# Kernel tuning notes

Hardware: AMD Instinct MI355X
Metric: run time of the kernel (lower is better)

## Reference

```python
import jax, jax.numpy as jnp
import numpy as np

N_NODES = 50000
N_EDGES = 1_600_000
D_IN, D_HID, D_OUT = 512, 256, 64


def setup_inputs() -> dict:
    key = jax.random.key(0)
    ks = jax.random.split(key, 8)
    x = jax.random.normal(ks[0], (N_NODES, D_IN), dtype=jnp.float32)
    edge_rows = jax.random.randint(ks[1], (N_EDGES,), 0, N_NODES, dtype=jnp.int32)
    edge_cols = jax.random.randint(ks[2], (N_EDGES,), 0, N_NODES, dtype=jnp.int32)
    # normalized adjacency values (e.g. D^-1/2 A D^-1/2 entries)
    edge_vals = jax.random.uniform(ks[3], (N_EDGES,), dtype=jnp.float32)
    W1 = jax.random.normal(ks[4], (D_IN, D_HID), dtype=jnp.float32) * (1.0 / np.sqrt(D_IN))
    b1 = jnp.zeros((D_HID,), dtype=jnp.float32)
    W2 = jax.random.normal(ks[5], (D_HID, D_OUT), dtype=jnp.float32) * (1.0 / np.sqrt(D_HID))
    b2 = jnp.zeros((D_OUT,), dtype=jnp.float32)
    return {"x": x, "edge_rows": edge_rows, "edge_cols": edge_cols,
            "edge_vals": edge_vals, "W1": W1, "b1": b1, "W2": W2, "b2": b2}


def _spmm(rows, cols, vals, h):
    # out[r] = sum_{e: rows[e]==r} vals[e] * h[cols[e]]
    msgs = vals[:, None] * h[cols]          # [E, d] gather
    return jax.ops.segment_sum(msgs, rows, num_segments=N_NODES)


def reference(x, edge_rows, edge_cols, edge_vals, W1, b1, W2, b2):
    h = x @ W1 + b1                          # W1(x)
    h = _spmm(edge_rows, edge_cols, edge_vals, h)  # sparse.mm(A_hat, h)
    h = jax.nn.relu(h)                       # relu; dropout is identity in eval
    h = h @ W2 + b2                           # W2(h)
    out = _spmm(edge_rows, edge_cols, edge_vals, h)
    return out
```

## Files before the change

kernel.cpp:

```cpp
#include <hip/hip_runtime.h>
#include <hip/hip_bf16.h>

constexpr int NN = 50000;
constexpr int NE = 1600000;
constexpr int DI = 512;
constexpr int DH = 256;
constexpr int DO = 64;

constexpr int NC = NN * 16;
constexpr int G1_BLOCKS = ((NN + 127) / 128) * (DH / 128);
constexpr int SC_BLOCKS = 2048;
constexpr int SCAN_BLOCKS = (NN + 1023) / 1024;
constexpr int E4_CAP = NE + NN * 16 + 64;

typedef __attribute__((ext_vector_type(8))) short short8;
typedef __attribute__((ext_vector_type(4))) float f32x4;

__device__ inline ushort f2b(float f) {
    uint u = __float_as_uint(f);
    u += 0x7fffu + ((u >> 16) & 1u);
    return (ushort)(u >> 16);
}
__device__ inline float b2f(ushort u) {
    return __uint_as_float((uint)u << 16);
}
__device__ inline void gload16(const void* g, void* l) {
    __builtin_amdgcn_global_load_lds(
        (const __attribute__((address_space(1))) unsigned int*)g,
        (__attribute__((address_space(3))) unsigned int*)l, 16, 0, 0);
}


__global__ void k_prep(const float* __restrict__ X, ushort* __restrict__ Xb,
                       const float* __restrict__ W1, ushort* __restrict__ w1bT,
                       const int* __restrict__ er, const int* __restrict__ ec,
                       int* __restrict__ counts2) {
    const int bid = blockIdx.x;
    const int tid = threadIdx.x;
    if (bid < 1024) {
        const float4* x4 = (const float4*)X;
        ushort4* o4 = (ushort4*)Xb;
        const int stride = 1024 * 256;
        for (int i = bid * 256 + tid; i < NN * DI / 4; i += stride) {
            float4 v = x4[i];
            o4[i] = make_ushort4(f2b(v.x), f2b(v.y), f2b(v.z), f2b(v.w));
        }
        for (int i = bid * 256 + tid; i < DI * DH; i += stride) {
            int n = i >> 9, k = i & 511;
            w1bT[i] = f2b(W1[(size_t)k * DH + n]);
        }
    } else {
        const int4* r4 = (const int4*)er;
        const int4* c4 = (const int4*)ec;
        const int stride = 1024 * 256;
        for (int i = (bid - 1024) * 256 + tid; i < NE / 4; i += stride) {
            int4 r = r4[i];
            int4 c = c4[i];
            atomicAdd(&counts2[(r.x << 4) | (c.x >> 12)], 1);
            atomicAdd(&counts2[(r.y << 4) | (c.y >> 12)], 1);
            atomicAdd(&counts2[(r.z << 4) | (c.z >> 12)], 1);
            atomicAdd(&counts2[(r.w << 4) | (c.w >> 12)], 1);
        }
    }
}


__global__ __launch_bounds__(1024) void k_scanA(const int* __restrict__ counts2,
                                                int* __restrict__ rp,
                                                int* __restrict__ partials) {
    const int t = threadIdx.x;
    const int r = blockIdx.x * 1024 + t;
    int s = 0;
    if (r < NN) {
        const int4* c4 = (const int4*)(counts2 + (size_t)r * 16);
        int4 a = c4[0], b = c4[1], c = c4[2], d = c4[3];
        s = a.x + a.y + a.z + a.w + b.x + b.y + b.z + b.w
          + c.x + c.y + c.z + c.w + d.x + d.y + d.z + d.w;
        s = (s + 15) & ~15;
    }
    __shared__ int buf[1024];
    buf[t] = s;
    __syncthreads();
    for (int off = 1; off < 1024; off <<= 1) {
        int v = (t >= off) ? buf[t - off] : 0;
        __syncthreads();
        buf[t] += v;
        __syncthreads();
    }
    if (r < NN) rp[r] = buf[t] - s;
    if (t == 1023) partials[blockIdx.x] = buf[1023];
}

__global__ __launch_bounds__(64) void k_scanB(int* __restrict__ partials,
                                              int* __restrict__ rp) {
    __shared__ int buf[64];
    int t = threadIdx.x;
    int v = (t < SCAN_BLOCKS) ? partials[t] : 0;
    buf[t] = v;
    __syncthreads();
    for (int off = 1; off < 64; off <<= 1) {
        int x = (t >= off) ? buf[t - off] : 0;
        __syncthreads();
        buf[t] += x;
        __syncthreads();
    }
    if (t < SCAN_BLOCKS) partials[t] = buf[t] - v;
    if (t == 63) rp[NN] = buf[63];
}

__global__ __launch_bounds__(1024) void k_scanC(const int* __restrict__ counts2,
                                                int* __restrict__ rp,
                                                int* __restrict__ cur2,
                                                const int* __restrict__ partials,
                                                const float* __restrict__ W2,
                                                ushort* __restrict__ w2bT) {
    const int t = threadIdx.x;
    const int r = blockIdx.x * 1024 + t;
    if (r < NN) {
        const int off = partials[blockIdx.x];
        const int base = rp[r] + off;
        rp[r] = base;
        const int4* c4 = (const int4*)(counts2 + (size_t)r * 16);
        int4 ca = c4[0], cb = c4[1], cc = c4[2], cd = c4[3];
        int cnt[16] = {ca.x, ca.y, ca.z, ca.w, cb.x, cb.y, cb.z, cb.w,
                       cc.x, cc.y, cc.z, cc.w, cd.x, cd.y, cd.z, cd.w};
        int out[16];
        int rs = 0;
        #pragma unroll
        for (int b = 0; b < 16; ++b) { out[b] = base + rs; rs += cnt[b]; }
        int4* o4 = (int4*)(cur2 + (size_t)r * 16);
        o4[0] = make_int4(out[0],  out[1],  out[2],  out[3]);
        o4[1] = make_int4(out[4],  out[5],  out[6],  out[7]);
        o4[2] = make_int4(out[8],  out[9],  out[10], out[11]);
        o4[3] = make_int4(out[12], out[13], out[14], out[15]);
    }
    if (blockIdx.x == 0) {
        for (int i = t; i < DH * DO; i += 1024) {
            int n = i >> 8, k = i & 255;
            w2bT[i] = f2b(W2[(size_t)k * DO + n]);
        }
    }
}


__global__ __launch_bounds__(256, 4) void k_gemm1(const ushort* __restrict__ Xb,
                                                  const ushort* __restrict__ w1bT,
                                                  const float* __restrict__ B,
                                                  ushort* __restrict__ H) {
    __shared__ ushort As[128 * 32];
    __shared__ ushort Bs[128 * 32];
    const int bid = blockIdx.x;
    const int bm = (bid >> 1) * 128;
    const int bn = (bid & 1) * 128;
    const int tid = threadIdx.x;
    const int wid = tid >> 6, lane = tid & 63;
    const int wm = wid >> 1, wn = wid & 1;
    const int lr = lane & 15, lg = lane >> 4;

    f32x4 acc[4][4];
    #pragma unroll
    for (int i = 0; i < 4; ++i)
        #pragma unroll
        for (int j = 0; j < 4; ++j)
            acc[i][j] = (f32x4){0.f, 0.f, 0.f, 0.f};

    for (int kt = 0; kt < DI; kt += 32) {
        #pragma unroll
        for (int c = 0; c < 2; ++c) {
            int i = c * 256 + tid;
            int row = i >> 2, slot = i & 3;
            const ushort* g = Xb + (size_t)(bm + row) * DI + kt + slot * 8;
            gload16(g, As + (size_t)(c * 256 + wid * 64) * 8);
        }
        #pragma unroll
        for (int c = 0; c < 2; ++c) {
            int i = c * 256 + tid;
            int row = i >> 2, slot = i & 3;
            const ushort* g = w1bT + (size_t)(bn + row) * DI + kt + slot * 8;
            gload16(g, Bs + (size_t)(c * 256 + wid * 64) * 8);
        }
        __syncthreads();

        short8 a[4], b[4];
        #pragma unroll
        for (int f = 0; f < 4; ++f) {
            a[f] = *(short8*)&As[(wm * 64 + f * 16 + lr) * 32 + lg * 8];
            b[f] = *(short8*)&Bs[(wn * 64 + f * 16 + lr) * 32 + lg * 8];
        }
        #pragma unroll
        for (int i = 0; i < 4; ++i)
            #pragma unroll
            for (int j = 0; j < 4; ++j)
                acc[i][j] = __builtin_amdgcn_mfma_f32_16x16x32_bf16(a[i], b[j], acc[i][j], 0, 0, 0);
        __syncthreads();
    }

    #pragma unroll
    for (int i = 0; i < 4; ++i) {
        int r0 = bm + wm * 64 + i * 16 + lg * 4;
        #pragma unroll
        for (int j = 0; j < 4; ++j) {
            int col = bn + wn * 64 + j * 16 + lr;
            float bias = B[col];
            #pragma unroll
            for (int e = 0; e < 4; ++e) {
                int r = r0 + e;
                if (r < NN) H[(size_t)r * DH + col] = f2b(acc[i][j][e] + bias);
            }
        }
    }
}


__global__ __launch_bounds__(256) void k_scatter(const int* __restrict__ er,
                                                 const int* __restrict__ ec,
                                                 const float* __restrict__ ev,
                                                 int* __restrict__ cur2,
                                                 uint* __restrict__ e4) {
    const int g = blockIdx.x & 7;
    const int lo = g * (NN / 8), hi = lo + (NN / 8);
    const int4* r4 = (const int4*)er;
    for (int q = (blockIdx.x >> 3) * 256 + (int)threadIdx.x; q < NE / 4;
         q += (SC_BLOCKS / 8) * 256) {
        int4 r = r4[q];
        #pragma unroll
        for (int e = 0; e < 4; ++e) {
            int rr = (e == 0) ? r.x : (e == 1) ? r.y : (e == 2) ? r.z : r.w;
            if (rr >= lo && rr < hi) {
                int c = ec[q * 4 + e];
                float v = ev[q * 4 + e];
                int p = atomicAdd(&cur2[(rr << 4) | (c >> 12)], 1);
                e4[p] = (uint)c | ((uint)f2b(v) << 16);
            }
        }
    }
}


__global__ __launch_bounds__(256) void k_srg(const int* __restrict__ rp,
                                             const uint* __restrict__ e4,
                                             const ushort* __restrict__ H,
                                             const ushort* __restrict__ w2bT,
                                             const float* __restrict__ B2,
                                             ushort* __restrict__ H2) {
    __shared__ ushort hs[16][264];
    const int tid = threadIdx.x;
    const int w = tid >> 6, lane = tid & 63;
    const int half = lane >> 5;
    const int dl = lane & 31;
    const ushort* gbase = H + dl * 8;
    const uint4* eq = (const uint4*)e4;

    #pragma unroll
    for (int q = 0; q < 4; ++q) {
        const int r = blockIdx.x * 16 + w * 4 + q;
        const int s = rp[r], e = rp[r + 1];
        float a[8] = {0.f, 0.f, 0.f, 0.f, 0.f, 0.f, 0.f, 0.f};

        int qi = s >> 2;
        uint4 q0 = eq[qi], q1 = eq[qi + 1], q2 = eq[qi + 2], q3 = eq[qi + 3];
        for (int i = s; i < e; i += 16) {
            uint u[8];
            u[0] = half ? q0.y : q0.x;  u[1] = half ? q0.w : q0.z;
            u[2] = half ? q1.y : q1.x;  u[3] = half ? q1.w : q1.z;
            u[4] = half ? q2.y : q2.x;  u[5] = half ? q2.w : q2.z;
            u[6] = half ? q3.y : q3.x;  u[7] = half ? q3.w : q3.z;
            uint4 hw[8];
            #pragma unroll
            for (int k = 0; k < 8; ++k)
                hw[k] = *(const uint4*)(gbase + (size_t)(u[k] & 0xffffu) * DH);
            qi += 4;
            q0 = eq[qi]; q1 = eq[qi + 1]; q2 = eq[qi + 2]; q3 = eq[qi + 3];
            #pragma unroll
            for (int k = 0; k < 8; ++k) {
                float v = __uint_as_float(u[k] & 0xffff0000u);
                uint w0 = hw[k].x, w1 = hw[k].y, w2 = hw[k].z, w3 = hw[k].w;
                a[0] += v * __uint_as_float(w0 << 16);
                a[1] += v * __uint_as_float(w0 & 0xffff0000u);
                a[2] += v * __uint_as_float(w1 << 16);
                a[3] += v * __uint_as_float(w1 & 0xffff0000u);
                a[4] += v * __uint_as_float(w2 << 16);
                a[5] += v * __uint_as_float(w2 & 0xffff0000u);
                a[6] += v * __uint_as_float(w3 << 16);
                a[7] += v * __uint_as_float(w3 & 0xffff0000u);
            }
        }
        #pragma unroll
        for (int d = 0; d < 8; ++d) a[d] += __shfl_xor(a[d], 32);
        if (half == 0) {
            short8 o;
            #pragma unroll
            for (int d = 0; d < 8; ++d) o[d] = (short)f2b(fmaxf(a[d], 0.f));
            *(short8*)&hs[w * 4 + q][dl * 8] = o;
        }
    }
    __syncthreads();

    const int lr = lane & 15, lg = lane >> 4;
    f32x4 acc = (f32x4){0.f, 0.f, 0.f, 0.f};
    #pragma unroll
    for (int kt = 0; kt < DH; kt += 32) {
        short8 af = *(short8*)&hs[lr][kt + lg * 8];
        short8 bf = *(const short8*)(w2bT + (size_t)(w * 16 + lr) * DH + kt + lg * 8);
        acc = __builtin_amdgcn_mfma_f32_16x16x32_bf16(af, bf, acc, 0, 0, 0);
    }
    const int col = w * 16 + lr;
    const float bias = B2[col];
    #pragma unroll
    for (int e = 0; e < 4; ++e) {
        int row = blockIdx.x * 16 + lg * 4 + e;
        H2[(size_t)row * DO + col] = f2b(acc[e] + bias);
    }
}


__global__ __launch_bounds__(256) void k_spmm_out(const int* __restrict__ rp,
                                                  const uint* __restrict__ e4,
                                                  const ushort* __restrict__ H2,
                                                  float* __restrict__ OUT) {
    const int seg = blockIdx.x & 3;
    const int r = (blockIdx.x >> 2) * 4 + (threadIdx.x >> 6);
    const int lane = threadIdx.x & 63;
    const int slot = lane >> 2;
    const int dq = lane & 3;
    const int s = rp[r], e = rp[r + 1];
    const ushort* base = H2 + seg * 16 + dq * 4;
    float a0 = 0.f, a1 = 0.f, a2 = 0.f, a3 = 0.f;

    for (int i = s + slot; i < e; i += 16) {
        uint u = e4[i];
        ushort4 h = *(const ushort4*)(base + (size_t)(u & 0xffffu) * DO);
        float v = __uint_as_float(u & 0xffff0000u);
        a0 += v * b2f(h.x); a1 += v * b2f(h.y); a2 += v * b2f(h.z); a3 += v * b2f(h.w);
    }
    #pragma unroll
    for (int m = 4; m < 64; m <<= 1) {
        a0 += __shfl_xor(a0, m); a1 += __shfl_xor(a1, m);
        a2 += __shfl_xor(a2, m); a3 += __shfl_xor(a3, m);
    }
    if (slot == 0) {
        *(float4*)(OUT + (size_t)r * DO + seg * 16 + dq * 4) = make_float4(a0, a1, a2, a3);
    }
}


extern "C" void kernel_launch(void* const* d_in, const int* in_sizes, int n_in,
                              void* d_out, int out_size, void* d_ws, size_t ws_size,
                              hipStream_t stream) {
    const float* x  = (const float*)d_in[0];
    const int*   er = (const int*)d_in[1];
    const int*   ec = (const int*)d_in[2];
    const float* ev = (const float*)d_in[3];
    const float* W1 = (const float*)d_in[4];
    const float* b1 = (const float*)d_in[5];
    const float* W2 = (const float*)d_in[6];
    const float* b2 = (const float*)d_in[7];
    float* out = (float*)d_out;

    char* ws = (char*)d_ws;
    ushort* Xb  = (ushort*)ws;
    uint*   e4  = (uint*)ws;   ws += (size_t)NN * DI * 2;
    ushort* h1  = (ushort*)ws; ws += (size_t)NN * DH * 2;
    ushort* h2  = (ushort*)ws; ws += (size_t)NN * DO * 2;
    int* counts2 = (int*)ws;   ws += ((size_t)NC * 4 + 255) & ~(size_t)255;
    int* rp     = (int*)ws;    ws += ((size_t)(NN + 1) * 4 + 255) & ~(size_t)255;
    int* cur2   = (int*)ws;    ws += ((size_t)NC * 4 + 255) & ~(size_t)255;
    int* partials = (int*)ws;  ws += 256;
    ushort* w1bT = (ushort*)ws; ws += ((size_t)DI * DH * 2 + 255) & ~(size_t)255;
    ushort* w2bT = (ushort*)ws; ws += ((size_t)DH * DO * 2 + 255) & ~(size_t)255;

    hipMemsetAsync(counts2, 0, (size_t)NC * 4, stream);
    k_prep<<<2048, 256, 0, stream>>>(x, Xb, W1, w1bT, er, ec, counts2);
    k_scanA<<<SCAN_BLOCKS, 1024, 0, stream>>>(counts2, rp, partials);
    k_scanB<<<1, 64, 0, stream>>>(partials, rp);
    k_scanC<<<SCAN_BLOCKS, 1024, 0, stream>>>(counts2, rp, cur2, partials, W2, w2bT);
    k_gemm1<<<G1_BLOCKS, 256, 0, stream>>>(Xb, w1bT, b1, h1);
    hipMemsetAsync(e4, 0, (size_t)E4_CAP * 4, stream);
    k_scatter<<<SC_BLOCKS, 256, 0, stream>>>(er, ec, ev, cur2, e4);
    k_srg<<<NN / 16, 256, 0, stream>>>(rp, e4, h1, w2bT, b2, h2);
    k_spmm_out<<<(NN / 4) * 4, 256, 0, stream>>>(rp, e4, h2, out);
}
```

Baseline: 378.5 us.

## Split fused SpMM+GEMM2 into column-segmented persistent SpMM and separate GEMM

Replaces the fused row-gather SpMM + relu + W2 MFMA kernel with a persistent SpMM that splits the 256 hidden columns into 8 segments across blocks, writing relu(h) to a bf16 buffer, followed by a standalone MFMA GEMM for W2. Grouping blocks by column segment is meant to shrink the per-pass gather working set so it fits better in cache, and to improve occupancy. The output SpMM likewise becomes persistent, with fixed row ranges per block group. The cost is an extra round trip through global memory for the intermediate, an extra launch, and rereading the edge list once per segment. The intermediate buffer is placed at a fixed offset inside the workspace region that e4 also lives in.

```diff
diff --git a/kernel.cpp b/kernel.cpp
--- a/kernel.cpp
+++ b/kernel.cpp
@@ -12,6 +12,14 @@
 constexpr int SC_BLOCKS = 2048;
 constexpr int SCAN_BLOCKS = (NN + 1023) / 1024;
 constexpr int E4_CAP = NE + NN * 16 + 64;
+
+constexpr int SP1_BLOCKS = 1024;
+constexpr int SP1_GROUPS = SP1_BLOCKS / 8;
+constexpr int SP1_RPG = (NN + SP1_GROUPS - 1) / SP1_GROUPS;
+
+constexpr int SP2_BLOCKS = 1024;
+constexpr int SP2_GROUPS = SP2_BLOCKS / 4;
+constexpr int SP2_RPG = (NN + SP2_GROUPS - 1) / SP2_GROUPS;
 
 typedef __attribute__((ext_vector_type(8))) short short8;
 typedef __attribute__((ext_vector_type(4))) float f32x4;
@@ -237,109 +245,128 @@
 }
 
 
-__global__ __launch_bounds__(256) void k_srg(const int* __restrict__ rp,
-                                             const uint* __restrict__ e4,
-                                             const ushort* __restrict__ H,
-                                             const ushort* __restrict__ w2bT,
-                                             const float* __restrict__ B2,
-                                             ushort* __restrict__ H2) {
-    __shared__ ushort hs[16][264];
+__global__ __launch_bounds__(256, 4) void k_spmm1p(const int* __restrict__ rp,
+                                                   const uint* __restrict__ e4,
+                                                   const ushort* __restrict__ H,
+                                                   ushort* __restrict__ O) {
+    const int seg = blockIdx.x & 7;
+    const int grp = blockIdx.x >> 3;
+    const int w = threadIdx.x >> 6, lane = threadIdx.x & 63;
+    const int slot = lane >> 3;
+    const int dq = lane & 7;
+    const ushort* gbase = H + seg * 32 + dq * 4;
+    const int r1 = min(grp * SP1_RPG + SP1_RPG, NN);
+
+    for (int r = grp * SP1_RPG + w; r < r1; r += 4) {
+        const int s = rp[r], e = rp[r + 1];
+        float a0 = 0.f, a1 = 0.f, a2 = 0.f, a3 = 0.f;
+        for (int i = s; i < e; i += 16) {
+            uint ua = e4[i + slot];
+            uint ub = e4[i + 8 + slot];
+            ushort4 ha = *(const ushort4*)(gbase + (size_t)(ua & 0xffffu) * DH);
+            ushort4 hb = *(const ushort4*)(gbase + (size_t)(ub & 0xffffu) * DH);
+            float va = __uint_as_float(ua & 0xffff0000u);
+            float vb = __uint_as_float(ub & 0xffff0000u);
+            a0 += va * b2f(ha.x) + vb * b2f(hb.x);
+            a1 += va * b2f(ha.y) + vb * b2f(hb.y);
+            a2 += va * b2f(ha.z) + vb * b2f(hb.z);
+            a3 += va * b2f(ha.w) + vb * b2f(hb.w);
+        }
+        #pragma unroll
+        for (int m = 8; m < 64; m <<= 1) {
+            a0 += __shfl_xor(a0, m); a1 += __shfl_xor(a1, m);
+            a2 += __shfl_xor(a2, m); a3 += __shfl_xor(a3, m);
+        }
+        if (slot == 0) {
+            ushort4 o = make_ushort4(f2b(fmaxf(a0, 0.f)), f2b(fmaxf(a1, 0.f)),
+                                     f2b(fmaxf(a2, 0.f)), f2b(fmaxf(a3, 0.f)));
+            *(ushort4*)(O + (size_t)r * DH + seg * 32 + dq * 4) = o;
+        }
+    }
+}
+
+
+__global__ __launch_bounds__(256) void k_gemm2(const ushort* __restrict__ HB,
+                                               const ushort* __restrict__ w2bT,
+                                               const float* __restrict__ B2,
+                                               ushort* __restrict__ H2) {
     const int tid = threadIdx.x;
-    const int w = tid >> 6, lane = tid & 63;
-    const int half = lane >> 5;
-    const int dl = lane & 31;
-    const ushort* gbase = H + dl * 8;
-    const uint4* eq = (const uint4*)e4;
-
+    const int wid = tid >> 6, lane = tid & 63;
+    const int lr = lane & 15, lg = lane >> 4;
+    const int r0 = blockIdx.x * 128 + wid * 32;
+
+    f32x4 acc[2][4];
     #pragma unroll
-    for (int q = 0; q < 4; ++q) {
-        const int r = blockIdx.x * 16 + w * 4 + q;
-        const int s = rp[r], e = rp[r + 1];
-        float a[8] = {0.f, 0.f, 0.f, 0.f, 0.f, 0.f, 0.f, 0.f};
-
-        int qi = s >> 2;
-        uint4 q0 = eq[qi], q1 = eq[qi + 1], q2 = eq[qi + 2], q3 = eq[qi + 3];
-        for (int i = s; i < e; i += 16) {
-            uint u[8];
-            u[0] = half ? q0.y : q0.x;  u[1] = half ? q0.w : q0.z;
-            u[2] = half ? q1.y : q1.x;  u[3] = half ? q1.w : q1.z;
-            u[4] = half ? q2.y : q2.x;  u[5] = half ? q2.w : q2.z;
-            u[6] = half ? q3.y : q3.x;  u[7] = half ? q3.w : q3.z;
-            uint4 hw[8];
+    for (int i = 0; i < 2; ++i)
+        #pragma unroll
+        for (int j = 0; j < 4; ++j)
+            acc[i][j] = (f32x4){0.f, 0.f, 0.f, 0.f};
+
+    for (int kt = 0; kt < DH; kt += 32) {
+        short8 a[2], b[4];
+        #pragma unroll
+        for (int f = 0; f < 2; ++f) {
+            int row = r0 + f * 16 + lr;
+            a[f] = (row < NN) ? *(const short8*)(HB + (size_t)row * DH + kt + lg * 8)
+                              : (short8){0,0,0,0,0,0,0,0};
+        }
+        #pragma unroll
+        for (int j = 0; j < 4; ++j)
+            b[j] = *(const short8*)(w2bT + (size_t)(j * 16 + lr) * DH + kt + lg * 8);
+        #pragma unroll
+        for (int i = 0; i < 2; ++i)
             #pragma unroll
-            for (int k = 0; k < 8; ++k)
-                hw[k] = *(const uint4*)(gbase + (size_t)(u[k] & 0xffffu) * DH);
-            qi += 4;
-            q0 = eq[qi]; q1 = eq[qi + 1]; q2 = eq[qi + 2]; q3 = eq[qi + 3];
+            for (int j = 0; j < 4; ++j)
+                acc[i][j] = __builtin_amdgcn_mfma_f32_16x16x32_bf16(a[i], b[j], acc[i][j], 0, 0, 0);
+    }
+
+    #pragma unroll
+    for (int i = 0; i < 2; ++i) {
+        #pragma unroll
+        for (int j = 0; j < 4; ++j) {
+            int col = j * 16 + lr;
+            float bias = B2[col];
             #pragma unroll
-            for (int k = 0; k < 8; ++k) {
-                float v = __uint_as_float(u[k] & 0xffff0000u);
-                uint w0 = hw[k].x, w1 = hw[k].y, w2 = hw[k].z, w3 = hw[k].w;
-                a[0] += v * __uint_as_float(w0 << 16);
-                a[1] += v * __uint_as_float(w0 & 0xffff0000u);
-                a[2] += v * __uint_as_float(w1 << 16);
-                a[3] += v * __uint_as_float(w1 & 0xffff0000u);
-                a[4] += v * __uint_as_float(w2 << 16);
-                a[5] += v * __uint_as_float(w2 & 0xffff0000u);
-                a[6] += v * __uint_as_float(w3 << 16);
-                a[7] += v * __uint_as_float(w3 & 0xffff0000u);
+            for (int e = 0; e < 4; ++e) {
+                int row = r0 + i * 16 + lg * 4 + e;
+                if (row < NN) H2[(size_t)row * DO + col] = f2b(acc[i][j][e] + bias);
             }
         }
-        #pragma unroll
-        for (int d = 0; d < 8; ++d) a[d] += __shfl_xor(a[d], 32);
-        if (half == 0) {
-            short8 o;
-            #pragma unroll
-            for (int d = 0; d < 8; ++d) o[d] = (short)f2b(fmaxf(a[d], 0.f));
-            *(short8*)&hs[w * 4 + q][dl * 8] = o;
-        }
-    }
-    __syncthreads();
-
-    const int lr = lane & 15, lg = lane >> 4;
-    f32x4 acc = (f32x4){0.f, 0.f, 0.f, 0.f};
-    #pragma unroll
-    for (int kt = 0; kt < DH; kt += 32) {
-        short8 af = *(short8*)&hs[lr][kt + lg * 8];
-        short8 bf = *(const short8*)(w2bT + (size_t)(w * 16 + lr) * DH + kt + lg * 8);
-        acc = __builtin_amdgcn_mfma_f32_16x16x32_bf16(af, bf, acc, 0, 0, 0);
-    }
-    const int col = w * 16 + lr;
-    const float bias = B2[col];
-    #pragma unroll
-    for (int e = 0; e < 4; ++e) {
-        int row = blockIdx.x * 16 + lg * 4 + e;
-        H2[(size_t)row * DO + col] = f2b(acc[e] + bias);
-    }
-}
-
-
-__global__ __launch_bounds__(256) void k_spmm_out(const int* __restrict__ rp,
-                                                  const uint* __restrict__ e4,
-                                                  const ushort* __restrict__ H2,
-                                                  float* __restrict__ OUT) {
+    }
+}
+
+
+__global__ __launch_bounds__(256, 4) void k_spmm_outp(const int* __restrict__ rp,
+                                                      const uint* __restrict__ e4,
+                                                      const ushort* __restrict__ H2,
+                                                      float* __restrict__ OUT) {
     const int seg = blockIdx.x & 3;
-    const int r = (blockIdx.x >> 2) * 4 + (threadIdx.x >> 6);
-    const int lane = threadIdx.x & 63;
+    const int grp = blockIdx.x >> 2;
+    const int w = threadIdx.x >> 6, lane = threadIdx.x & 63;
     const int slot = lane >> 2;
     const int dq = lane & 3;
-    const int s = rp[r], e = rp[r + 1];
-    const ushort* base = H2 + seg * 16 + dq * 4;
-    float a0 = 0.f, a1 = 0.f, a2 = 0.f, a3 = 0.f;
-
-    for (int i = s + slot; i < e; i += 16) {
-        uint u = e4[i];
-        ushort4 h = *(const ushort4*)(base + (size_t)(u & 0xffffu) * DO);
-        float v = __uint_as_float(u & 0xffff0000u);
-        a0 += v * b2f(h.x); a1 += v * b2f(h.y); a2 += v * b2f(h.z); a3 += v * b2f(h.w);
-    }
-    #pragma unroll
-    for (int m = 4; m < 64; m <<= 1) {
-        a0 += __shfl_xor(a0, m); a1 += __shfl_xor(a1, m);
-        a2 += __shfl_xor(a2, m); a3 += __shfl_xor(a3, m);
-    }
-    if (slot == 0) {
-        *(float4*)(OUT + (size_t)r * DO + seg * 16 + dq * 4) = make_float4(a0, a1, a2, a3);
+    const ushort* gbase = H2 + seg * 16 + dq * 4;
+    const int r1 = min(grp * SP2_RPG + SP2_RPG, NN);
+
+    for (int r = grp * SP2_RPG + w; r < r1; r += 4) {
+        const int s = rp[r], e = rp[r + 1];
+        float a0 = 0.f, a1 = 0.f, a2 = 0.f, a3 = 0.f;
+        for (int i = s; i < e; i += 16) {
+            uint u = e4[i + slot];
+            ushort4 h = *(const ushort4*)(gbase + (size_t)(u & 0xffffu) * DO);
+            float v = __uint_as_float(u & 0xffff0000u);
+            a0 += v * b2f(h.x); a1 += v * b2f(h.y);
+            a2 += v * b2f(h.z); a3 += v * b2f(h.w);
+        }
+        #pragma unroll
+        for (int m = 4; m < 64; m <<= 1) {
+            a0 += __shfl_xor(a0, m); a1 += __shfl_xor(a1, m);
+            a2 += __shfl_xor(a2, m); a3 += __shfl_xor(a3, m);
+        }
+        if (slot == 0) {
+            *(float4*)(OUT + (size_t)r * DO + seg * 16 + dq * 4) =
+                make_float4(a0, a1, a2, a3);
+        }
     }
 }
 
@@ -359,7 +386,9 @@
 
     char* ws = (char*)d_ws;
     ushort* Xb  = (ushort*)ws;
-    uint*   e4  = (uint*)ws;   ws += (size_t)NN * DI * 2;
+    uint*   e4  = (uint*)ws;
+    ushort* h1b = (ushort*)(ws + (size_t)12 * 1024 * 1024);
+    ws += (size_t)NN * DI * 2;
     ushort* h1  = (ushort*)ws; ws += (size_t)NN * DH * 2;
     ushort* h2  = (ushort*)ws; ws += (size_t)NN * DO * 2;
     int* counts2 = (int*)ws;   ws += ((size_t)NC * 4 + 255) & ~(size_t)255;
@@ -377,6 +406,7 @@
     k_gemm1<<<G1_BLOCKS, 256, 0, stream>>>(Xb, w1bT, b1, h1);
     hipMemsetAsync(e4, 0, (size_t)E4_CAP * 4, stream);
     k_scatter<<<SC_BLOCKS, 256, 0, stream>>>(er, ec, ev, cur2, e4);
-    k_srg<<<NN / 16, 256, 0, stream>>>(rp, e4, h1, w2bT, b2, h2);
-    k_spmm_out<<<(NN / 4) * 4, 256, 0, stream>>>(rp, e4, h2, out);
-}
+    k_spmm1p<<<SP1_BLOCKS, 256, 0, stream>>>(rp, e4, h1, h1b);
+    k_gemm2<<<(NN + 127) / 128, 256, 0, stream>>>(h1b, w2bT, b2, h2);
+    k_spmm_outp<<<SP2_BLOCKS, 256, 0, stream>>>(rp, e4, h2, out);
+}
```

Measured after the change: 556.4 us. 47.0% more time.

## Pack row/col indices for scatter and widen output SpMM gathers

Applied to the files above, without the earlier changes.

k_prep now also writes each edge's row and column as one packed 32-bit word. k_scatter reads that packed array instead of separate row and column arrays, which removes the per-edge column reads from its eight-way partitioned passes. k_spmm_out is restructured to one block per four rows, each wave covering all 64 output features. Each lane handles eight features and two edges per iteration, using 16-byte bf16 gathers and a uint2 edge load. This relies on row padding in the edge buffer (zero entries) and on uint2 alignment of row starts, and the packing assumes node ids fit in 16 bits.

```diff
diff --git a/kernel.cpp b/kernel.cpp
--- a/kernel.cpp
+++ b/kernel.cpp
@@ -34,7 +34,7 @@
 __global__ void k_prep(const float* __restrict__ X, ushort* __restrict__ Xb,
                        const float* __restrict__ W1, ushort* __restrict__ w1bT,
                        const int* __restrict__ er, const int* __restrict__ ec,
-                       int* __restrict__ counts2) {
+                       int* __restrict__ counts2, uint* __restrict__ rc32) {
     const int bid = blockIdx.x;
     const int tid = threadIdx.x;
     if (bid < 1024) {
@@ -56,6 +56,9 @@
         for (int i = (bid - 1024) * 256 + tid; i < NE / 4; i += stride) {
             int4 r = r4[i];
             int4 c = c4[i];
+            *(uint4*)&rc32[i * 4] = make_uint4(
+                ((uint)r.x << 16) | (uint)c.x, ((uint)r.y << 16) | (uint)c.y,
+                ((uint)r.z << 16) | (uint)c.z, ((uint)r.w << 16) | (uint)c.w);
             atomicAdd(&counts2[(r.x << 4) | (c.x >> 12)], 1);
             atomicAdd(&counts2[(r.y << 4) | (c.y >> 12)], 1);
             atomicAdd(&counts2[(r.z << 4) | (c.z >> 12)], 1);
@@ -212,25 +215,25 @@
 }
 
 
-__global__ __launch_bounds__(256) void k_scatter(const int* __restrict__ er,
-                                                 const int* __restrict__ ec,
+__global__ __launch_bounds__(256) void k_scatter(const uint* __restrict__ rc32,
                                                  const float* __restrict__ ev,
                                                  int* __restrict__ cur2,
                                                  uint* __restrict__ e4) {
     const int g = blockIdx.x & 7;
-    const int lo = g * (NN / 8), hi = lo + (NN / 8);
-    const int4* r4 = (const int4*)er;
+    const uint lo = g * (NN / 8), hi = lo + (NN / 8);
+    const uint4* rc4 = (const uint4*)rc32;
     for (int q = (blockIdx.x >> 3) * 256 + (int)threadIdx.x; q < NE / 4;
          q += (SC_BLOCKS / 8) * 256) {
-        int4 r = r4[q];
+        uint4 t = rc4[q];
         #pragma unroll
         for (int e = 0; e < 4; ++e) {
-            int rr = (e == 0) ? r.x : (e == 1) ? r.y : (e == 2) ? r.z : r.w;
+            uint rc = (e == 0) ? t.x : (e == 1) ? t.y : (e == 2) ? t.z : t.w;
+            uint rr = rc >> 16;
             if (rr >= lo && rr < hi) {
-                int c = ec[q * 4 + e];
+                uint c = rc & 0xffffu;
                 float v = ev[q * 4 + e];
                 int p = atomicAdd(&cur2[(rr << 4) | (c >> 12)], 1);
-                e4[p] = (uint)c | ((uint)f2b(v) << 16);
+                e4[p] = c | ((uint)f2b(v) << 16);
             }
         }
     }
@@ -318,28 +321,34 @@
                                                   const uint* __restrict__ e4,
                                                   const ushort* __restrict__ H2,
                                                   float* __restrict__ OUT) {
-    const int seg = blockIdx.x & 3;
-    const int r = (blockIdx.x >> 2) * 4 + (threadIdx.x >> 6);
+    const int r = blockIdx.x * 4 + (threadIdx.x >> 6);
     const int lane = threadIdx.x & 63;
-    const int slot = lane >> 2;
-    const int dq = lane & 3;
+    const int slot = lane >> 3;
+    const int dq = lane & 7;
     const int s = rp[r], e = rp[r + 1];
-    const ushort* base = H2 + seg * 16 + dq * 4;
-    float a0 = 0.f, a1 = 0.f, a2 = 0.f, a3 = 0.f;
-
-    for (int i = s + slot; i < e; i += 16) {
-        uint u = e4[i];
-        ushort4 h = *(const ushort4*)(base + (size_t)(u & 0xffffu) * DO);
-        float v = __uint_as_float(u & 0xffff0000u);
-        a0 += v * b2f(h.x); a1 += v * b2f(h.y); a2 += v * b2f(h.z); a3 += v * b2f(h.w);
-    }
-    #pragma unroll
-    for (int m = 4; m < 64; m <<= 1) {
-        a0 += __shfl_xor(a0, m); a1 += __shfl_xor(a1, m);
-        a2 += __shfl_xor(a2, m); a3 += __shfl_xor(a3, m);
+    const ushort* base = H2 + dq * 8;
+    float a[8] = {0.f, 0.f, 0.f, 0.f, 0.f, 0.f, 0.f, 0.f};
+
+    for (int i = s; i < e; i += 16) {
+        uint2 u = *(const uint2*)(e4 + i + 2 * slot);
+        short8 h0 = *(const short8*)(base + (size_t)(u.x & 0xffffu) * DO);
+        short8 h1 = *(const short8*)(base + (size_t)(u.y & 0xffffu) * DO);
+        float v0 = __uint_as_float(u.x & 0xffff0000u);
+        float v1 = __uint_as_float(u.y & 0xffff0000u);
+        #pragma unroll
+        for (int d = 0; d < 8; ++d)
+            a[d] += v0 * b2f((ushort)h0[d]) + v1 * b2f((ushort)h1[d]);
+    }
+    #pragma unroll
+    for (int d = 0; d < 8; ++d) {
+        a[d] += __shfl_xor(a[d], 8);
+        a[d] += __shfl_xor(a[d], 16);
+        a[d] += __shfl_xor(a[d], 32);
     }
     if (slot == 0) {
-        *(float4*)(OUT + (size_t)r * DO + seg * 16 + dq * 4) = make_float4(a0, a1, a2, a3);
+        float* o = OUT + (size_t)r * DO + dq * 8;
+        *(float4*)o       = make_float4(a[0], a[1], a[2], a[3]);
+        *(float4*)(o + 4) = make_float4(a[4], a[5], a[6], a[7]);
     }
 }
 
@@ -359,9 +368,11 @@
 
     char* ws = (char*)d_ws;
     ushort* Xb  = (ushort*)ws;
-    uint*   e4  = (uint*)ws;   ws += (size_t)NN * DI * 2;
+    uint*   e4  = (uint*)ws;
+    ws += (size_t)NN * DI * 2;
     ushort* h1  = (ushort*)ws; ws += (size_t)NN * DH * 2;
-    ushort* h2  = (ushort*)ws; ws += (size_t)NN * DO * 2;
+    ushort* h2  = (ushort*)ws;
+    uint*   rc32 = (uint*)ws;  ws += (size_t)NN * DO * 2;
     int* counts2 = (int*)ws;   ws += ((size_t)NC * 4 + 255) & ~(size_t)255;
     int* rp     = (int*)ws;    ws += ((size_t)(NN + 1) * 4 + 255) & ~(size_t)255;
     int* cur2   = (int*)ws;    ws += ((size_t)NC * 4 + 255) & ~(size_t)255;
@@ -370,13 +381,13 @@
     ushort* w2bT = (ushort*)ws; ws += ((size_t)DH * DO * 2 + 255) & ~(size_t)255;
 
     hipMemsetAsync(counts2, 0, (size_t)NC * 4, stream);
-    k_prep<<<2048, 256, 0, stream>>>(x, Xb, W1, w1bT, er, ec, counts2);
+    k_prep<<<2048, 256, 0, stream>>>(x, Xb, W1, w1bT, er, ec, counts2, rc32);
     k_scanA<<<SCAN_BLOCKS, 1024, 0, stream>>>(counts2, rp, partials);
     k_scanB<<<1, 64, 0, stream>>>(partials, rp);
     k_scanC<<<SCAN_BLOCKS, 1024, 0, stream>>>(counts2, rp, cur2, partials, W2, w2bT);
     k_gemm1<<<G1_BLOCKS, 256, 0, stream>>>(Xb, w1bT, b1, h1);
     hipMemsetAsync(e4, 0, (size_t)E4_CAP * 4, stream);
-    k_scatter<<<SC_BLOCKS, 256, 0, stream>>>(er, ec, ev, cur2, e4);
+    k_scatter<<<SC_BLOCKS, 256, 0, stream>>>(rc32, ev, cur2, e4);
     k_srg<<<NN / 16, 256, 0, stream>>>(rp, e4, h1, w2bT, b2, h2);
-    k_spmm_out<<<(NN / 4) * 4, 256, 0, stream>>>(rp, e4, h2, out);
-}
+    k_spmm_out<<<NN / 4, 256, 0, stream>>>(rp, e4, h2, out);
+}
```

Result: faster. 328.5 us (-13.2%).
